# Optimization experiments

Hardware: AMD Instinct MI355X
Metric: run time of the kernel (lower is better)

The kernel has to match this reference:

```python
import math
import jax, jax.numpy as jnp
import numpy as np

SCALE = 4; K = 7; R = 3; K2 = K * K
BANDS = 10; FEAT = 64; HID = 256; HEADS = 4
LH = 96; LW = 96; H = LH * SCALE; W = LW * SCALE
IN_DIM = FEAT + 4 * BANDS + 2  # 106
REF_HID = 48  # 3 groups * 16


def _conv(x, w, b, groups=1):
    y = jax.lax.conv_general_dilated(x, w, (1, 1), 'SAME',
        dimension_numbers=('NCHW', 'OIHW', 'NCHW'), feature_group_count=groups)
    return y + b[None, :, None, None]


def _gelu(x):
    return jax.nn.gelu(x, approximate=False)  # torch nn.GELU default (erf)


def _gray(x):  # [B,3,H,W] -> [B,1,H,W]
    return 0.2989 * x[:, 0:1] + 0.587 * x[:, 1:2] + 0.114 * x[:, 2:3]


def setup_inputs() -> dict:
    key = jax.random.key(0)
    ks = iter(jax.random.split(key, 64))
    def W_(sh, s=0.05):
        return (jax.random.normal(next(ks), sh, dtype=jnp.float32) * s)
    def Z_(sh):
        return jnp.zeros(sh, jnp.float32)
    d = {}
    d['lr'] = jax.random.uniform(next(ks), (1, 3, LH, LW), dtype=jnp.float32)
    d['enc_w0'] = W_((FEAT, 3, 3, 3)); d['enc_b0'] = Z_((FEAT,))
    d['enc_w1'] = W_((FEAT, FEAT, 3, 3)); d['enc_b1'] = Z_((FEAT,))
    d['enc_w2'] = W_((FEAT, FEAT, 3, 3)); d['enc_b2'] = Z_((FEAT,))
    d['enc_w3'] = W_((FEAT, FEAT, 3, 3)); d['enc_b3'] = Z_((FEAT,))
    # cond_fuser: 1x1 convs, cond_ch=2 (hover bnd+mask, zeros at inference)
    d['cond_w0'] = W_((FEAT, FEAT + 2, 1, 1)); d['cond_b0'] = Z_((FEAT,))
    d['cond_w1'] = W_((FEAT, FEAT, 1, 1)); d['cond_b1'] = Z_((FEAT,))
    # KernelMLP backbone: 5 Linear layers
    d['mlp_w0'] = W_((IN_DIM, HID)); d['mlp_b0'] = Z_((HID,))
    d['mlp_w1'] = W_((HID, HID)); d['mlp_b1'] = Z_((HID,))
    d['mlp_w2'] = W_((HID, HID)); d['mlp_b2'] = Z_((HID,))
    d['mlp_w3'] = W_((HID, HID)); d['mlp_b3'] = Z_((HID,))
    d['mlp_w4'] = W_((HID, HID)); d['mlp_b4'] = Z_((HID,))
    d['hk_w'] = W_((HID, HEADS * K2)); d['hk_b'] = Z_((HEADS * K2,))
    d['hg_w'] = W_((HID, HEADS)); d['hg_b'] = Z_((HEADS,))
    # ResidualRefiner: grouped convs, groups=3 (OIHW with in/groups channels)
    d['ref_w0'] = W_((REF_HID, 2, 3, 3)); d['ref_b0'] = Z_((REF_HID,))
    d['ref_w1'] = W_((REF_HID, 16, 3, 3)); d['ref_b1'] = Z_((REF_HID,))
    d['ref_w2'] = W_((3, 16, 3, 3)); d['ref_b2'] = Z_((3,))
    return d


def reference(lr, enc_w0, enc_b0, enc_w1, enc_b1, enc_w2, enc_b2, enc_w3, enc_b3,
              cond_w0, cond_b0, cond_w1, cond_b1,
              mlp_w0, mlp_b0, mlp_w1, mlp_b1, mlp_w2, mlp_b2, mlp_w3, mlp_b3,
              mlp_w4, mlp_b4, hk_w, hk_b, hg_w, hg_b,
              ref_w0, ref_b0, ref_w1, ref_b1, ref_w2, ref_b2):
    # --- local CNN features on LR grid ---
    f = _gelu(_conv(lr, enc_w0, enc_b0))
    f = _gelu(_conv(f, enc_w1, enc_b1))
    f = _gelu(_conv(f, enc_w2, enc_b2))
    f = _gelu(_conv(f, enc_w3, enc_b3))
    cond = jnp.zeros((1, 2, LH, LW), f.dtype)  # no hover maps at inference
    f = _conv(jnp.concatenate([f, cond], axis=1), cond_w0, cond_b0)
    f = _conv(_gelu(f), cond_w1, cond_b1)
    # --- bilinear upsample (align_corners=False semantics) ---
    lr_up = jax.image.resize(lr, (1, 3, H, W), method='bilinear')
    # --- HR pixel grid -> LR centers + fractional offsets ---
    yy, xx = jnp.meshgrid(jnp.arange(H), jnp.arange(W), indexing='ij')
    xx = xx.reshape(-1).astype(jnp.float32)
    yy = yy.reshape(-1).astype(jnp.float32)
    lx = (xx + 0.5) / SCALE - 0.5
    ly = (yy + 0.5) / SCALE - 0.5
    cx = jnp.clip(jnp.round(lx), 0, LW - 1)
    cy = jnp.clip(jnp.round(ly), 0, LH - 1)
    dx = (lx - cx)[:, None]
    dy = (ly - cy)[:, None]
    cxi = cx.astype(jnp.int32)
    cyi = cy.astype(jnp.int32)
    idx = cyi * LW + cxi  # flattened gather index [N]
    feat_flat = f[0].reshape(FEAT, -1).T  # [lh*lw, FEAT]
    cf = feat_flat[idx]                   # [N, FEAT]
    # --- Fourier PE of normalized HR coords ---
    xn = (xx + 0.5) / W * 2.0 - 1.0
    yn = (yy + 0.5) / H * 2.0 - 1.0
    freq = (2.0 ** jnp.arange(BANDS, dtype=jnp.float32)) * math.pi
    ax = xn[:, None] * freq[None, :]
    ay = yn[:, None] * freq[None, :]
    pe = jnp.stack([jnp.sin(ax), jnp.cos(ax), jnp.sin(ay), jnp.cos(ay)], axis=-1)
    pe = pe.reshape(-1, 4 * BANDS)  # per-band [sinx,cosx,siny,cosy] order
    # --- per-pixel kernel MLP ---
    z = jnp.concatenate([cf, pe, dx, dy], axis=1)  # [N, 106]
    h = _gelu(z @ mlp_w0 + mlp_b0)
    h = _gelu(h @ mlp_w1 + mlp_b1)
    h = _gelu(h @ mlp_w2 + mlp_b2)
    h = _gelu(h @ mlp_w3 + mlp_b3)
    h = _gelu(h @ mlp_w4 + mlp_b4)
    klog = (h @ hk_w + hk_b).reshape(-1, HEADS, K2)
    glog = h @ hg_w + hg_b
    ker = jax.nn.softmax(klog, axis=-1)   # non-negative kernels
    gate = jax.nn.softmax(glog, axis=-1)  # head mixture
    kmix = jnp.einsum('nh,nhk->nk', gate, ker)  # [N, K2]
    # --- gather KxK LR neighborhood and apply adaptive kernel ---
    oy, ox = jnp.meshgrid(jnp.arange(-R, R + 1), jnp.arange(-R, R + 1), indexing='ij')
    ox = ox.reshape(-1); oy = oy.reshape(-1)  # offsets: oy outer, ox inner
    nx = jnp.clip(cxi[:, None] + ox[None, :], 0, LW - 1)
    ny = jnp.clip(cyi[:, None] + oy[None, :], 0, LH - 1)
    nidx = ny * LW + nx                     # [N, K2]
    lr_flat = lr[0].reshape(3, -1).T        # [lh*lw, 3]
    patches = lr_flat[nidx]                 # [N, K2, 3]
    pred = jnp.einsum('nk,nkc->nc', kmix, patches)  # [N, 3]
    sr = pred.reshape(H, W, 3).transpose(2, 0, 1)[None]  # [1,3,H,W]
    # --- color-safe residual refiner (groups=3) ---
    res0 = sr - lr_up
    x6 = jnp.concatenate([lr_up, res0], axis=1)
    r1 = _gelu(_conv(x6, ref_w0, ref_b0, groups=3))
    r1 = _gelu(_conv(r1, ref_w1, ref_b1, groups=3))
    res = _conv(r1, ref_w2, ref_b2, groups=3)
    sr2 = sr + res
    # --- color-preserving fusion: inject only grayscale residual ---
    delta = _gray(sr2) - _gray(lr_up)
    out = jnp.clip(lr_up + delta, 0.0, 1.0)
    return out
```

## Files before the change

### kernel.cpp

```cpp
#include <hip/hip_runtime.h>
#include <math.h>

#define LWI 96
#define LHI 96
#define HWD 384
#define NPIX 147456
#define LRPIX 9216
#define HID 256

typedef __attribute__((ext_vector_type(8))) _Float16 f16x8;
typedef __attribute__((ext_vector_type(4))) _Float16 f16x4;
typedef __attribute__((ext_vector_type(16))) float f32x16;

__device__ __forceinline__ float gelu_fast(float x){
  float x2 = x*x;
  float u = x*(-2.3021181f - 0.1029443f*x2);
  float e = exp2f(u);
  return x * __builtin_amdgcn_rcpf(1.0f + e);
}

__device__ __forceinline__ float lr_up_at(const float* __restrict__ lr, int c, int y, int x){
  float sy = (y+0.5f)*0.25f - 0.5f;
  float sx = (x+0.5f)*0.25f - 0.5f;
  float fy = floorf(sy), fx = floorf(sx);
  float ty = sy - fy, tx = sx - fx;
  int y0 = (int)fy, x0 = (int)fx;
  int y0c = min(max(y0,0),LHI-1), y1c = min(max(y0+1,0),LHI-1);
  int x0c = min(max(x0,0),LWI-1), x1c = min(max(x0+1,0),LWI-1);
  const float* p = lr + c*LRPIX;
  float v00 = p[y0c*LWI+x0c], v01 = p[y0c*LWI+x1c];
  float v10 = p[y1c*LWI+x0c], v11 = p[y1c*LWI+x1c];
  return (1.f-ty)*((1.f-tx)*v00 + tx*v01) + ty*((1.f-tx)*v10 + tx*v11);
}

__global__ __launch_bounds__(256) void conv3x3_f16out(
    const float* __restrict__ in, const float* __restrict__ w,
    const float* __restrict__ b, _Float16* __restrict__ out16){
  int tid = blockIdx.x*256 + threadIdx.x;
  int o = tid / LRPIX; int rem = tid - o*LRPIX;
  int y = rem / LWI;   int x = rem - y*LWI;
  int ou = __builtin_amdgcn_readfirstlane(o);
  float acc = b[ou];
  const float* wo = w + ou*27;
  for (int i=0;i<3;++i){
    const float* inp = in + i*LRPIX;
    #pragma unroll
    for (int dy=0;dy<3;++dy){
      int yy = y + dy - 1;
      bool yok = (yy>=0 && yy<LHI);
      #pragma unroll
      for (int dx=0;dx<3;++dx){
        int xx = x + dx - 1;
        float v = (yok && xx>=0 && xx<LWI) ? inp[yy*LWI+xx] : 0.0f;
        acc = fmaf(wo[i*9 + dy*3 + dx], v, acc);
      }
    }
  }
  out16[rem*64 + o] = (_Float16)gelu_fast(acc);
}

__global__ __launch_bounds__(256) void pack_convw(
  const float* __restrict__ cw1, const float* __restrict__ cw2,
  const float* __restrict__ cw3, _Float16* __restrict__ WC)
{
  int i = blockIdx.x*256 + threadIdx.x;
  if (i >= 110592) return;
  int cv = i / 36864; int s2 = i - cv*36864;
  int tkf = s2 >> 9; int s = s2 & 511;
  int tap = tkf >> 3; int ksfb = tkf & 7;
  int ks = ksfb >> 1; int fb = ksfb & 1;
  int slot = s >> 3; int e = s & 7;
  int oc = fb*32 + (slot & 31);
  int ic = ks*16 + (slot>>5)*8 + e;
  int dy = tap/3, dx = tap - (tap/3)*3;
  const float* src = (cv==0)?cw1:(cv==1)?cw2:cw3;
  WC[i] = (_Float16)src[((oc*64+ic)*3+dy)*3+dx];
}

__global__ __launch_bounds__(256) void conv_mfma_kernel(
    const _Float16* __restrict__ Xin, const _Float16* __restrict__ WC,
    const float* __restrict__ bias, _Float16* __restrict__ Xout, int cv)
{
  __shared__ _Float16 xs[100*64];
  __shared__ float red[2][2][64][20];
  const int t = threadIdx.x;
  const int lane = t & 63;
  const int w = __builtin_amdgcn_readfirstlane(t >> 6);
  const int fb = w & 1, kh = w >> 1;
  const int g = lane >> 5;
  const int gx0 = blockIdx.x*8, gy0 = blockIdx.y*8;

  for (int i = t; i < 800; i += 256){
    int sp = i >> 3, c = i & 7;
    int ly = (sp*205)>>11; int lx = sp - ly*10;
    int gy = gy0 - 1 + ly, gx = gx0 - 1 + lx;
    f16x8 v = f16x8{};
    if (gy>=0 && gy<LHI && gx>=0 && gx<LWI)
      v = *(const f16x8*)(Xin + (gy*LWI+gx)*64 + c*8);
    *(f16x8*)(xs + sp*64 + ((c ^ (sp&7))*8)) = v;
  }
  __syncthreads();

  const _Float16* WCc = WC + cv*36864;
  const int p0 = lane & 31;
  const int py0 = p0 >> 3, px0 = p0 & 7;
  f32x16 acc0{}, acc1{};
  #pragma unroll
  for (int tap = 0; tap < 9; ++tap){
    const int dy = tap/3, dx = tap - (tap/3)*3;
    #pragma unroll
    for (int ksl = 0; ksl < 2; ++ksl){
      int ks = kh*2 + ksl;
      f16x8 A = *(const f16x8*)(WCc + ((tap*4+ks)*2+fb)*512 + lane*8);
      int sp0 = (py0+dy)*10 + (px0+dx);
      int sp1 = (py0+4+dy)*10 + (px0+dx);
      int c0 = ks*2 + g;
      f16x8 B0 = *(const f16x8*)(xs + sp0*64 + ((c0 ^ (sp0&7))*8));
      f16x8 B1 = *(const f16x8*)(xs + sp1*64 + ((c0 ^ (sp1&7))*8));
      acc0 = __builtin_amdgcn_mfma_f32_32x32x16_f16(A,B0,acc0,0,0,0);
      acc1 = __builtin_amdgcn_mfma_f32_32x32x16_f16(A,B1,acc1,0,0,0);
    }
  }
  if (kh == 1){
    #pragma unroll
    for (int r4=0;r4<4;++r4){
      float4 v0 = make_float4(acc0[r4*4],acc0[r4*4+1],acc0[r4*4+2],acc0[r4*4+3]);
      float4 v1 = make_float4(acc1[r4*4],acc1[r4*4+1],acc1[r4*4+2],acc1[r4*4+3]);
      *(float4*)&red[fb][0][lane][r4*4] = v0;
      *(float4*)&red[fb][1][lane][r4*4] = v1;
    }
  }
  __syncthreads();
  if (kh == 0){
    #pragma unroll
    for (int ph=0; ph<2; ++ph){
      const f32x16& acc = ph ? acc1 : acc0;
      int py = ph*4 + py0;
      int gpx = (gy0+py)*LWI + (gx0+px0);
      #pragma unroll
      for (int r4=0;r4<4;++r4){
        float4 rr = *(const float4*)&red[fb][ph][lane][r4*4];
        float4 bb = *(const float4*)&bias[fb*32 + 8*r4 + 4*g];
        f16x4 o;
        o[0] = (_Float16)gelu_fast(acc[r4*4+0] + rr.x + bb.x);
        o[1] = (_Float16)gelu_fast(acc[r4*4+1] + rr.y + bb.y);
        o[2] = (_Float16)gelu_fast(acc[r4*4+2] + rr.z + bb.z);
        o[3] = (_Float16)gelu_fast(acc[r4*4+3] + rr.w + bb.w);
        *(f16x4*)(Xout + gpx*64 + fb*32 + 8*r4 + 4*g) = o;
      }
    }
  }
}

__global__ __launch_bounds__(256) void conv1x1_f16(
    const _Float16* __restrict__ in16, const float* __restrict__ w,
    const float* __restrict__ b, _Float16* __restrict__ out16,
    int wstride, int dogelu){
  int tid = blockIdx.x*256 + threadIdx.x;
  int o = tid / LRPIX; int p = tid - o*LRPIX;
  int ou = __builtin_amdgcn_readfirstlane(o);
  float acc = b[ou];
  const float* wo = w + ou*wstride;
  const _Float16* ip = in16 + p*64;
  f16x8 iv[8];
  #pragma unroll
  for (int q=0;q<8;++q) iv[q] = *(const f16x8*)(ip + q*8);
  #pragma unroll
  for (int q=0;q<8;++q)
    #pragma unroll
    for (int j=0;j<8;++j)
      acc = fmaf(wo[q*8+j], (float)iv[q][j], acc);
  out16[p*64 + o] = (_Float16)(dogelu ? gelu_fast(acc) : acc);
}

__global__ __launch_bounds__(256) void pack_weights(
  const float* __restrict__ mw0, const float* __restrict__ mw1,
  const float* __restrict__ mw2, const float* __restrict__ mw3,
  const float* __restrict__ mw4, const float* __restrict__ hkw,
  const float* __restrict__ hgw,
  const float* __restrict__ mb0, const float* __restrict__ mb1,
  const float* __restrict__ mb2, const float* __restrict__ mb3,
  const float* __restrict__ mb4, const float* __restrict__ hkb,
  const float* __restrict__ hgb,
  _Float16* __restrict__ WB, float* __restrict__ biasAll)
{
  int i = blockIdx.x*256 + threadIdx.x;
  if (i < 356352){
    int layer, local;
    if (i < 28672){ layer = 0; local = i; }
    else { layer = 1 + ((i-28672)>>16); local = (i-28672)&65535; }
    int ks = local >> 12; int r = local & 4095;
    int cb = r >> 9; int s2 = r & 511; int slot = s2 >> 3; int e = s2 & 7;
    int col = cb*32 + (slot & 31); int g = slot >> 5;
    int k = ks*16 + g*8 + e;
    float v = 0.f;
    if (layer == 0){ if (k < 106) v = mw0[k*256+col]; }
    else if (layer == 1) v = mw1[k*256+col];
    else if (layer == 2) v = mw2[k*256+col];
    else if (layer == 3) v = mw3[k*256+col];
    else if (layer == 4) v = mw4[k*256+col];
    else { if (col < 196) v = hkw[k*196+col]; else if (col < 200) v = hgw[k*4+col-196]; }
    WB[i] = (_Float16)v;
  } else if (i < 356352+1536){
    int j = i - 356352; int layer = j>>8; int col = j&255;
    float v = 0.f;
    if (layer==0) v=mb0[col]; else if (layer==1) v=mb1[col]; else if(layer==2) v=mb2[col];
    else if(layer==3) v=mb3[col]; else if(layer==4) v=mb4[col];
    else { if (col<196) v=hkb[col]; else if(col<200) v=hgb[col-196]; }
    biasAll[j] = v;
  }
}

template<int NKS>
__device__ __forceinline__ void mlp_pass(const _Float16* __restrict__ Wl,
    const _Float16* __restrict__ buf, int lane, int w, f32x16 (&acc)[2]){
  acc[0] = f32x16{}; acc[1] = f32x16{};
  #pragma unroll
  for (int ks=0; ks<NKS; ++ks){
    f16x8 a = *(const f16x8*)(Wl + (ks*8+w)*512 + lane*8);
    const _Float16* bp = buf + ks*1024 + lane*8;
    f16x8 b0 = *(const f16x8*)(bp);
    f16x8 b1 = *(const f16x8*)(bp + 512);
    acc[0] = __builtin_amdgcn_mfma_f32_32x32x16_f16(a,b0,acc[0],0,0,0);
    acc[1] = __builtin_amdgcn_mfma_f32_32x32x16_f16(a,b1,acc[1],0,0,0);
  }
}

__global__ __launch_bounds__(512,6) void mlp_mfma3_kernel(
  const _Float16* __restrict__ feat16, const float* __restrict__ lr,
  const _Float16* __restrict__ WB, const float* __restrict__ biasAll,
  float* __restrict__ sr)
{
  __shared__ _Float16 buf[16384];
  const int t = threadIdx.x;
  const int lane = t & 63;
  const int w = __builtin_amdgcn_readfirstlane(t >> 6);
  const int p31 = lane & 31; const int hi = lane >> 5;

  {
    const int p = lane; const int q = w;
    const int px = blockIdx.x*64 + p;
    const int y = px / HWD; const int x = px - y*HWD;
    float lx = (x+0.5f)*0.25f - 0.5f;
    float ly = (y+0.5f)*0.25f - 0.5f;
    float cxf = fminf(fmaxf(rintf(lx),0.f),95.f);
    float cyf = fminf(fmaxf(rintf(ly),0.f),95.f);
    int base = (int)cyf*LWI + (int)cxf;
    auto zwrite = [&](int k, float v){
      buf[((k>>4)*2 + (p>>5))*512 + ((p&31) + 32*((k>>3)&1))*8 + (k&7)] = (_Float16)v;
    };
    auto zwriteh = [&](int k, _Float16 v){
      buf[((k>>4)*2 + (p>>5))*512 + ((p&31) + 32*((k>>3)&1))*8 + (k&7)] = v;
    };
    if (q < 2){
      const _Float16* fsrc = feat16 + base*64 + q*32;
      #pragma unroll
      for (int j=0;j<32;++j) zwriteh(q*32+j, fsrc[j]);
    } else if (q == 2){
      float xn = (x+0.5f)/384.0f*2.0f - 1.0f;
      float s = sinf(xn*3.14159265358979323846f);
      float c = cosf(xn*3.14159265358979323846f);
      #pragma unroll
      for (int b=0;b<10;++b){
        zwrite(64+4*b+0, s); zwrite(64+4*b+1, c);
        float s2 = 2.f*s*c; float c2 = 1.f - 2.f*s*s;
        s=s2; c=c2;
      }
      zwrite(104, lx-cxf); zwrite(105, ly-cyf);
    } else if (q == 3){
      float yn = (y+0.5f)/384.0f*2.0f - 1.0f;
      float s = sinf(yn*3.14159265358979323846f);
      float c = cosf(yn*3.14159265358979323846f);
      #pragma unroll
      for (int b=0;b<10;++b){
        zwrite(64+4*b+2, s); zwrite(64+4*b+3, c);
        float s2 = 2.f*s*c; float c2 = 1.f - 2.f*s*s;
        s=s2; c=c2;
      }
    } else if (q == 4){
      #pragma unroll
      for (int k=106;k<112;++k) zwrite(k, 0.f);
    }
  }
  __syncthreads();

  #pragma unroll 1
  for (int L=0; L<5; ++L){
    static const int WOFFS[5] = {0,28672,94208,159744,225280};
    f32x16 acc[2];
    if (L==0) mlp_pass<7>(WB, buf, lane, w, acc);
    else      mlp_pass<16>(WB + WOFFS[L], buf, lane, w, acc);
    __syncthreads();
    const float* Bl = biasAll + L*256;
    #pragma unroll
    for (int q2=0;q2<4;++q2){
      float4 bs = *(const float4*)&Bl[w*32 + q2*8 + 4*hi];
      const float* bp2 = (const float*)&bs;
      int ks2 = w*2 + (q2>>1); int g2 = q2&1;
      _Float16* dst = buf + (ks2*2)*512 + (p31 + 32*g2)*8 + 4*hi;
      #pragma unroll
      for (int pb=0;pb<2;++pb){
        f16x4 o;
        #pragma unroll
        for (int r=0;r<4;++r) o[r] = (_Float16)gelu_fast(acc[pb][q2*4+r] + bp2[r]);
        *(f16x4*)(dst + pb*512) = o;
      }
    }
    __syncthreads();
  }

  {
    f32x16 acc[2];
    if (w < 7) mlp_pass<16>(WB + 290816, buf, lane, w, acc);
    __syncthreads();
    if (w < 7){
      #pragma unroll
      for (int reg=0;reg<16;++reg){
        int f = w*32 + (reg&3) + 8*(reg>>2) + 4*hi;
        if (f < 200){
          float bias = biasAll[1280 + f];
          buf[f*72 + p31]      = (_Float16)(acc[0][reg] + bias);
          buf[f*72 + 32 + p31] = (_Float16)(acc[1][reg] + bias);
        }
      }
    }
  }
  __syncthreads();

  if (t < 256){
    const int p = t & 63; const int hd = t >> 6;
    auto KL = [&](int col)->float { return (float)buf[col*72 + p]; };
    const float L2E = 1.4426950408889634f;
    float g0=KL(196),g1=KL(197),g2=KL(198),g3=KL(199);
    float gm = fmaxf(fmaxf(g0,g1),fmaxf(g2,g3));
    float e0=exp2f((g0-gm)*L2E),e1=exp2f((g1-gm)*L2E),
          e2=exp2f((g2-gm)*L2E),e3=exp2f((g3-gm)*L2E);
    float gate = ((hd==0)?e0:(hd==1)?e1:(hd==2)?e2:e3)/(e0+e1+e2+e3);
    float m = -1e30f;
    #pragma unroll
    for (int k=0;k<49;++k) m = fmaxf(m, KL(hd*49+k));
    float s = 0.f;
    float ev[49];
    #pragma unroll
    for (int k=0;k<49;++k){ float e=exp2f((KL(hd*49+k)-m)*L2E); s+=e; ev[k]=e; }
    float sc = gate/s;
    #pragma unroll
    for (int k=0;k<49;++k) buf[(hd*49+k)*72 + p] = (_Float16)(ev[k]*sc);
  }
  __syncthreads();

  if (t < 192){
    const int c = t >> 6; const int p = t & 63;
    const int px = blockIdx.x*64 + p;
    const int y = px / HWD; const int x = px - y*HWD;
    float lx = (x+0.5f)*0.25f - 0.5f;
    float ly = (y+0.5f)*0.25f - 0.5f;
    int cxi = (int)fminf(fmaxf(rintf(lx),0.f),95.f);
    int cyi = (int)fminf(fmaxf(rintf(ly),0.f),95.f);
    const float* lrc = lr + c*LRPIX;
    float acc = 0.f;
    #pragma unroll
    for (int k=0;k<49;++k){
      float km = (float)buf[k*72+p] + (float)buf[(49+k)*72+p]
               + (float)buf[(98+k)*72+p] + (float)buf[(147+k)*72+p];
      int oy = k/7 - 3, ox = k - (k/7)*7 - 3;
      int nyy = min(max(cyi+oy,0),95), nxx = min(max(cxi+ox,0),95);
      acc = fmaf(km, lrc[nyy*LWI+nxx], acc);
    }
    sr[c*NPIX + px] = acc;
  }
}

__global__ __launch_bounds__(256) void refiner_group_kernel(
  const float* __restrict__ lr, const float* __restrict__ srg,
  const float* __restrict__ w0, const float* __restrict__ b0,
  const float* __restrict__ w1, const float* __restrict__ b1,
  const float* __restrict__ w2, const float* __restrict__ b2,
  float* __restrict__ resW)
{
  __shared__ float x6s[2][22][26];
  __shared__ float r1a[16][20][20];
  __shared__ float r1b[16][18][20];
  const int g = blockIdx.z;
  const int tid = threadIdx.x;
  const int gx0 = blockIdx.x*16, gy0 = blockIdx.y*16;

  for (int i = tid; i < 2*22*22; i += 256){
    int ic = i / 484; int rem = i - ic*484; int yy = rem / 22; int xx = rem - yy*22;
    int ch = g*2 + ic;
    int gy = gy0 - 3 + yy, gx = gx0 - 3 + xx;
    float v = 0.f;
    if (gy>=0 && gy<HWD && gx>=0 && gx<HWD){
      int c = (ch<3)?ch:(ch-3);
      float lu = lr_up_at(lr, c, gy, gx);
      v = (ch < 3) ? lu : (srg[c*NPIX + gy*HWD + gx] - lu);
    }
    x6s[ic][yy][xx] = v;
  }
  __syncthreads();

  for (int task = tid; task < 320; task += 256){
    int o = task / 20; int yy = task - o*20;
    int og = g*16 + o;
    float bias = b0[og];
    float acc[20];
    #pragma unroll
    for (int j=0;j<20;++j) acc[j] = bias;
    #pragma unroll
    for (int ic=0; ic<2; ++ic){
      #pragma unroll
      for (int dyy=0; dyy<3; ++dyy){
        float row[22];
        #pragma unroll
        for (int j=0;j<22;++j) row[j] = x6s[ic][yy+dyy][j];
        #pragma unroll
        for (int dxx=0; dxx<3; ++dxx){
          float wv = w0[((og*2+ic)*3+dyy)*3+dxx];
          #pragma unroll
          for (int j=0;j<20;++j) acc[j] = fmaf(wv, row[j+dxx], acc[j]);
        }
      }
    }
    int gyy = gy0 - 2 + yy;
    bool rok = (gyy>=0 && gyy<HWD);
    #pragma unroll
    for (int j=0;j<20;++j){
      int gxx = gx0 - 2 + j;
      r1a[o][yy][j] = (rok && gxx>=0 && gxx<HWD) ? gelu_fast(acc[j]) : 0.f;
    }
  }
  __syncthreads();

  for (int task = tid; task < 288; task += 256){
    int o = task / 18; int yy = task - o*18;
    int og = g*16 + o;
    float bias = b1[og];
    float acc[18];
    #pragma unroll
    for (int j=0;j<18;++j) acc[j] = bias;
    for (int ic=0; ic<16; ++ic){
      #pragma unroll
      for (int dyy=0; dyy<3; ++dyy){
        float row[20];
        #pragma unroll
        for (int q=0;q<5;++q)
          *(float4*)&row[q*4] = *(const float4*)&r1a[ic][yy+dyy][q*4];
        #pragma unroll
        for (int dxx=0; dxx<3; ++dxx){
          float wv = w1[((og*16+ic)*3+dyy)*3+dxx];
          #pragma unroll
          for (int j=0;j<18;++j) acc[j] = fmaf(wv, row[j+dxx], acc[j]);
        }
      }
    }
    int gyy = gy0 - 1 + yy;
    bool rok = (gyy>=0 && gyy<HWD);
    #pragma unroll
    for (int j=0;j<18;++j){
      int gxx = gx0 - 1 + j;
      r1b[o][yy][j] = (rok && gxx>=0 && gxx<HWD) ? gelu_fast(acc[j]) : 0.f;
    }
  }
  __syncthreads();

  {
    int ty = tid >> 4, tx = tid & 15;
    float a = b2[g];
    for (int ic=0; ic<16; ++ic){
      #pragma unroll
      for (int dyy=0; dyy<3; ++dyy){
        #pragma unroll
        for (int dxx=0; dxx<3; ++dxx){
          a = fmaf(w2[((g*16+ic)*3+dyy)*3+dxx], r1b[ic][ty+dyy][tx+dxx], a);
        }
      }
    }
    resW[g*NPIX + (gy0+ty)*HWD + gx0+tx] = a;
  }
}

__global__ __launch_bounds__(256) void fuse_kernel(
  const float* __restrict__ lr, const float* __restrict__ srg,
  const float* __restrict__ resW, float* __restrict__ out)
{
  int p = blockIdx.x*256 + threadIdx.x;
  int y = p / HWD, x = p - y*HWD;
  float lu[3];
  float d = 0.f;
  const float cf0=0.2989f, cf1=0.587f, cf2=0.114f;
  lu[0] = lr_up_at(lr, 0, y, x);
  lu[1] = lr_up_at(lr, 1, y, x);
  lu[2] = lr_up_at(lr, 2, y, x);
  d += cf0*(srg[0*NPIX+p] + resW[0*NPIX+p] - lu[0]);
  d += cf1*(srg[1*NPIX+p] + resW[1*NPIX+p] - lu[1]);
  d += cf2*(srg[2*NPIX+p] + resW[2*NPIX+p] - lu[2]);
  #pragma unroll
  for (int c=0;c<3;++c){
    float o_ = lu[c] + d;
    out[c*NPIX + p] = fminf(fmaxf(o_, 0.f), 1.f);
  }
}

extern "C" void kernel_launch(void* const* d_in, const int* in_sizes, int n_in,
                              void* d_out, int out_size, void* d_ws, size_t ws_size,
                              hipStream_t stream){
  const float* lr  = (const float*)d_in[0];
  const float* ew0 = (const float*)d_in[1];  const float* eb0 = (const float*)d_in[2];
  const float* ew1 = (const float*)d_in[3];  const float* eb1 = (const float*)d_in[4];
  const float* ew2 = (const float*)d_in[5];  const float* eb2 = (const float*)d_in[6];
  const float* ew3 = (const float*)d_in[7];  const float* eb3 = (const float*)d_in[8];
  const float* cw0 = (const float*)d_in[9];  const float* cb0 = (const float*)d_in[10];
  const float* cw1 = (const float*)d_in[11]; const float* cb1 = (const float*)d_in[12];
  const float* mw0 = (const float*)d_in[13]; const float* mb0 = (const float*)d_in[14];
  const float* mw1 = (const float*)d_in[15]; const float* mb1 = (const float*)d_in[16];
  const float* mw2 = (const float*)d_in[17]; const float* mb2 = (const float*)d_in[18];
  const float* mw3 = (const float*)d_in[19]; const float* mb3 = (const float*)d_in[20];
  const float* mw4 = (const float*)d_in[21]; const float* mb4 = (const float*)d_in[22];
  const float* hkw = (const float*)d_in[23]; const float* hkb = (const float*)d_in[24];
  const float* hgw = (const float*)d_in[25]; const float* hgb = (const float*)d_in[26];
  const float* rw0 = (const float*)d_in[27]; const float* rb0 = (const float*)d_in[28];
  const float* rw1 = (const float*)d_in[29]; const float* rb1 = (const float*)d_in[30];
  const float* rw2 = (const float*)d_in[31]; const float* rb2 = (const float*)d_in[32];

  float* ws = (float*)d_ws;
  _Float16* X0 = (_Float16*)ws;
  _Float16* X1 = (_Float16*)(ws + 294912);
  float* srp   = ws + 589824;
  _Float16* WB = (_Float16*)(ws + 1032192);
  _Float16* WC = (_Float16*)(ws + 1210368);
  float* biasAll = ws + 1265664;
  float* resW  = ws + 1267200;

  pack_weights<<<1398,256,0,stream>>>(mw0,mw1,mw2,mw3,mw4,hkw,hgw,
      mb0,mb1,mb2,mb3,mb4,hkb,hgb, WB, biasAll);
  pack_convw<<<432,256,0,stream>>>(ew1, ew2, ew3, WC);

  conv3x3_f16out<<<2304,256,0,stream>>>(lr, ew0, eb0, X0);
  conv_mfma_kernel<<<dim3(12,12),256,0,stream>>>(X0, WC, eb1, X1, 0);
  conv_mfma_kernel<<<dim3(12,12),256,0,stream>>>(X1, WC, eb2, X0, 1);
  conv_mfma_kernel<<<dim3(12,12),256,0,stream>>>(X0, WC, eb3, X1, 2);
  conv1x1_f16<<<2304,256,0,stream>>>(X1, cw0, cb0, X0, 66, 1);
  conv1x1_f16<<<2304,256,0,stream>>>(X0, cw1, cb1, X1, 64, 0);

  mlp_mfma3_kernel<<<2304,512,0,stream>>>(X1, lr, WB, biasAll, srp);

  refiner_group_kernel<<<dim3(24,24,3),256,0,stream>>>(lr, srp,
      rw0,rb0, rw1,rb1, rw2,rb2, resW);
  fuse_kernel<<<576,256,0,stream>>>(lr, srp, resW, (float*)d_out);
}
```

Measured before the change: 345.8 us.

## Use MFMA for 1x1 cond convs and precombine head kernels in gather

Replaces the scalar per-output-channel 1x1 conv kernels with an MFMA-based kernel that stages 64 pixels in shared memory and multiplies against prepacked fp16 weights. The weights are packed in the existing conv-weight pack kernel, which now also covers the 1x1 layers. In the MLP kernel, the four head kernels are summed once into shared memory before the gather, and interior pixels use an unclamped fast path for the neighbourhood loads. The fp16 rounding of the mixed kernel and the extra syncs trade a little precision and sync cost for fewer reads and less arithmetic.

After: 324.0 us. -6.3%, faster.

```diff
diff --git a/kernel.cpp b/kernel.cpp
--- a/kernel.cpp
+++ b/kernel.cpp
@@ -61,20 +61,31 @@
 
 __global__ __launch_bounds__(256) void pack_convw(
   const float* __restrict__ cw1, const float* __restrict__ cw2,
-  const float* __restrict__ cw3, _Float16* __restrict__ WC)
+  const float* __restrict__ cw3, const float* __restrict__ xw0,
+  const float* __restrict__ xw1,
+  _Float16* __restrict__ WC, _Float16* __restrict__ WX)
 {
   int i = blockIdx.x*256 + threadIdx.x;
-  if (i >= 110592) return;
-  int cv = i / 36864; int s2 = i - cv*36864;
-  int tkf = s2 >> 9; int s = s2 & 511;
-  int tap = tkf >> 3; int ksfb = tkf & 7;
-  int ks = ksfb >> 1; int fb = ksfb & 1;
-  int slot = s >> 3; int e = s & 7;
-  int oc = fb*32 + (slot & 31);
-  int ic = ks*16 + (slot>>5)*8 + e;
-  int dy = tap/3, dx = tap - (tap/3)*3;
-  const float* src = (cv==0)?cw1:(cv==1)?cw2:cw3;
-  WC[i] = (_Float16)src[((oc*64+ic)*3+dy)*3+dx];
+  if (i < 110592){
+    int cv = i / 36864; int s2 = i - cv*36864;
+    int tkf = s2 >> 9; int s = s2 & 511;
+    int tap = tkf >> 3; int ksfb = tkf & 7;
+    int ks = ksfb >> 1; int fb = ksfb & 1;
+    int slot = s >> 3; int e = s & 7;
+    int oc = fb*32 + (slot & 31);
+    int ic = ks*16 + (slot>>5)*8 + e;
+    int dy = tap/3, dx = tap - (tap/3)*3;
+    const float* src = (cv==0)?cw1:(cv==1)?cw2:cw3;
+    WC[i] = (_Float16)src[((oc*64+ic)*3+dy)*3+dx];
+  } else if (i < 118784){
+    int j = i - 110592;
+    int cv = j >> 12; int s2 = j & 4095;
+    int ks = s2 >> 10; int fb = (s2 >> 9) & 1; int s = s2 & 511;
+    int slot = s >> 3; int e = s & 7;
+    int oc = fb*32 + (slot & 31);
+    int ic = ks*16 + (slot>>5)*8 + e;
+    WX[j] = (_Float16)((cv==0) ? xw0[oc*66+ic] : xw1[oc*64+ic]);
+  }
 }
 
 __global__ __launch_bounds__(256) void conv_mfma_kernel(
@@ -152,25 +163,45 @@
   }
 }
 
-__global__ __launch_bounds__(256) void conv1x1_f16(
-    const _Float16* __restrict__ in16, const float* __restrict__ w,
-    const float* __restrict__ b, _Float16* __restrict__ out16,
-    int wstride, int dogelu){
-  int tid = blockIdx.x*256 + threadIdx.x;
-  int o = tid / LRPIX; int p = tid - o*LRPIX;
-  int ou = __builtin_amdgcn_readfirstlane(o);
-  float acc = b[ou];
-  const float* wo = w + ou*wstride;
-  const _Float16* ip = in16 + p*64;
-  f16x8 iv[8];
+__global__ __launch_bounds__(256) void conv1x1_mfma(
+    const _Float16* __restrict__ Xin, const _Float16* __restrict__ W1,
+    const float* __restrict__ bias, _Float16* __restrict__ Xout, int dogelu)
+{
+  __shared__ _Float16 bufB[4096];
+  const int t = threadIdx.x;
+  const int lane = t & 63;
+  const int w = __builtin_amdgcn_readfirstlane(t >> 6);
+  const int fb = w & 1, ph = w >> 1;
+  const int px0 = blockIdx.x * 64;
   #pragma unroll
-  for (int q=0;q<8;++q) iv[q] = *(const f16x8*)(ip + q*8);
+  for (int h = 0; h < 2; ++h){
+    int i = t + h*256;
+    int p = i & 63, c = i >> 6;
+    f16x8 v = *(const f16x8*)(Xin + (px0+p)*64 + c*8);
+    *(f16x8*)(bufB + ((c>>1)*2 + (p>>5))*512 + ((p&31)+32*(c&1))*8) = v;
+  }
+  __syncthreads();
+  f32x16 acc{};
   #pragma unroll
-  for (int q=0;q<8;++q)
-    #pragma unroll
-    for (int j=0;j<8;++j)
-      acc = fmaf(wo[q*8+j], (float)iv[q][j], acc);
-  out16[p*64 + o] = (_Float16)(dogelu ? gelu_fast(acc) : acc);
+  for (int ks=0; ks<4; ++ks){
+    f16x8 A = *(const f16x8*)(W1 + (ks*2+fb)*512 + lane*8);
+    f16x8 B = *(const f16x8*)(bufB + (ks*2+ph)*512 + lane*8);
+    acc = __builtin_amdgcn_mfma_f32_32x32x16_f16(A,B,acc,0,0,0);
+  }
+  const int p31 = lane & 31, hi = lane >> 5;
+  int px = px0 + ph*32 + p31;
+  #pragma unroll
+  for (int q=0;q<4;++q){
+    float4 bb = *(const float4*)&bias[fb*32 + q*8 + 4*hi];
+    const float* bp = (const float*)&bb;
+    f16x4 o;
+    #pragma unroll
+    for (int r=0;r<4;++r){
+      float v = acc[q*4+r] + bp[r];
+      o[r] = (_Float16)(dogelu ? gelu_fast(v) : v);
+    }
+    *(f16x4*)(Xout + px*64 + fb*32 + q*8 + 4*hi) = o;
+  }
 }
 
 __global__ __launch_bounds__(256) void pack_weights(
@@ -349,6 +380,29 @@
   }
   __syncthreads();
 
+  {
+    float kv[7];
+    #pragma unroll
+    for (int j=0;j<7;++j){
+      int i = t + j*512;
+      if (i < 3136){
+        int k = i >> 6, p = i & 63;
+        kv[j] = (float)buf[k*72+p] + (float)buf[(49+k)*72+p]
+              + (float)buf[(98+k)*72+p] + (float)buf[(147+k)*72+p];
+      }
+    }
+    __syncthreads();
+    #pragma unroll
+    for (int j=0;j<7;++j){
+      int i = t + j*512;
+      if (i < 3136){
+        int k = i >> 6, p = i & 63;
+        buf[k*72+p] = (_Float16)kv[j];
+      }
+    }
+  }
+  __syncthreads();
+
   if (t < 192){
     const int c = t >> 6; const int p = t & 63;
     const int px = blockIdx.x*64 + p;
@@ -359,13 +413,22 @@
     int cyi = (int)fminf(fmaxf(rintf(ly),0.f),95.f);
     const float* lrc = lr + c*LRPIX;
     float acc = 0.f;
-    #pragma unroll
-    for (int k=0;k<49;++k){
-      float km = (float)buf[k*72+p] + (float)buf[(49+k)*72+p]
-               + (float)buf[(98+k)*72+p] + (float)buf[(147+k)*72+p];
-      int oy = k/7 - 3, ox = k - (k/7)*7 - 3;
-      int nyy = min(max(cyi+oy,0),95), nxx = min(max(cxi+ox,0),95);
-      acc = fmaf(km, lrc[nyy*LWI+nxx], acc);
+    bool interior = (cxi>=3 && cxi<=92 && cyi>=3 && cyi<=92);
+    if (__all(interior)){
+      const float* lrb = lrc + (cyi-3)*LWI + (cxi-3);
+      #pragma unroll
+      for (int k=0;k<49;++k){
+        float km = (float)buf[k*72+p];
+        acc = fmaf(km, lrb[(k/7)*LWI + (k - (k/7)*7)], acc);
+      }
+    } else {
+      #pragma unroll
+      for (int k=0;k<49;++k){
+        float km = (float)buf[k*72+p];
+        int oy = k/7 - 3, ox = k - (k/7)*7 - 3;
+        int nyy = min(max(cyi+oy,0),95), nxx = min(max(cxi+ox,0),95);
+        acc = fmaf(km, lrc[nyy*LWI+nxx], acc);
+      }
     }
     sr[c*NPIX + px] = acc;
   }
@@ -530,17 +593,18 @@
   _Float16* WC = (_Float16*)(ws + 1210368);
   float* biasAll = ws + 1265664;
   float* resW  = ws + 1267200;
+  _Float16* WX = (_Float16*)(ws + 1709568);
 
   pack_weights<<<1398,256,0,stream>>>(mw0,mw1,mw2,mw3,mw4,hkw,hgw,
       mb0,mb1,mb2,mb3,mb4,hkb,hgb, WB, biasAll);
-  pack_convw<<<432,256,0,stream>>>(ew1, ew2, ew3, WC);
+  pack_convw<<<464,256,0,stream>>>(ew1, ew2, ew3, cw0, cw1, WC, WX);
 
   conv3x3_f16out<<<2304,256,0,stream>>>(lr, ew0, eb0, X0);
   conv_mfma_kernel<<<dim3(12,12),256,0,stream>>>(X0, WC, eb1, X1, 0);
   conv_mfma_kernel<<<dim3(12,12),256,0,stream>>>(X1, WC, eb2, X0, 1);
   conv_mfma_kernel<<<dim3(12,12),256,0,stream>>>(X0, WC, eb3, X1, 2);
-  conv1x1_f16<<<2304,256,0,stream>>>(X1, cw0, cb0, X0, 66, 1);
-  conv1x1_f16<<<2304,256,0,stream>>>(X0, cw1, cb1, X1, 64, 0);
+  conv1x1_mfma<<<144,256,0,stream>>>(X1, WX,        cb0, X0, 1);
+  conv1x1_mfma<<<144,256,0,stream>>>(X0, WX + 4096, cb1, X1, 0);
 
   mlp_mfma3_kernel<<<2304,512,0,stream>>>(X1, lr, WB, biasAll, srp);
 
```
